# Optimization experiments

Hardware: AMD Instinct MI355X
Metric: run time of the kernel (lower is better)

## Reference

```python
import jax, jax.numpy as jnp
import numpy as np

SEQ, BATCH = 512, 32
VOCAB, HID, FF = 32000, 1024, 4096
HEADS, NX, MAXLEN = 8, 6, 512
EPS = 1e-5


def _full_layer_norm(t):
    # F.layer_norm(t, t.shape): normalize over ALL elements, no affine
    m = jnp.mean(t)
    v = jnp.mean((t - m) ** 2)
    return (t - m) * jax.lax.rsqrt(v + EPS)


def _attention(x, wq, bq, wk, bk, wv, bv, wo, bo):
    # x: [S, B, H]; faithful to the module's quirky reshape:
    # view(B, S//heads, heads, H) splits the SEQUENCE dim across heads,
    # each head keeps the full feature dim H; scores scaled by sqrt(H//heads).
    S, B, H = x.shape
    head_dim = H // HEADS
    q = x @ wq + bq
    k = x @ wk + bk
    v = x @ wv + bv

    def split(t):  # [S,B,H] -> [B, heads, S//heads, H]
        return t.transpose(1, 0, 2).reshape(B, S // HEADS, HEADS, H).transpose(0, 2, 1, 3)

    qh, kh, vh = split(q), split(k), split(v)
    energy = jnp.einsum('bhtf,bhsf->bhts', qh, kh) / np.sqrt(head_dim)
    att = jax.nn.softmax(energy, axis=-1)          # [B, heads, S//h, S//h]
    va = jnp.einsum('bhts,bhsf->bhtf', att, vh)    # [B, heads, S//h, H]
    va = va.transpose(2, 0, 1, 3).reshape(S, B, H)  # back to [S, B, H]
    return va @ wo + bo


def _sub_encoder(x, p, i):
    a = _attention(x, p['wq'][i], p['bq'][i], p['wk'][i], p['bk'][i],
                   p['wv'][i], p['bv'][i], p['wo'][i], p['bo'][i])
    mid = _full_layer_norm(a + x)
    f = jax.nn.relu(mid @ p['w1'][i] + p['b1'][i]) @ p['w2'][i] + p['b2'][i]
    return _full_layer_norm(mid + f)


def setup_inputs() -> dict:
    key = jax.random.key(0)
    ks = jax.random.split(key, 16)
    s = 0.02
    inp = {
        'x': jax.random.randint(ks[0], (SEQ, BATCH), 0, VOCAB),
        'emb': jax.random.normal(ks[1], (VOCAB, HID), jnp.float32) * s,
        'pos_emb': jax.random.normal(ks[2], (MAXLEN, HID), jnp.float32) * s,
        'wq': jax.random.normal(ks[3], (NX, HID, HID), jnp.float32) * s,
        'bq': jnp.zeros((NX, HID), jnp.float32),
        'wk': jax.random.normal(ks[4], (NX, HID, HID), jnp.float32) * s,
        'bk': jnp.zeros((NX, HID), jnp.float32),
        'wv': jax.random.normal(ks[5], (NX, HID, HID), jnp.float32) * s,
        'bv': jnp.zeros((NX, HID), jnp.float32),
        'wo': jax.random.normal(ks[6], (NX, HID, HID), jnp.float32) * s,
        'bo': jnp.zeros((NX, HID), jnp.float32),
        'w1': jax.random.normal(ks[7], (NX, HID, FF), jnp.float32) * s,
        'b1': jnp.zeros((NX, FF), jnp.float32),
        'w2': jax.random.normal(ks[8], (NX, FF, HID), jnp.float32) * s,
        'b2': jnp.zeros((NX, HID), jnp.float32),
    }
    return inp


def reference(x, emb, pos_emb, wq, bq, wk, bk, wv, bv, wo, bo, w1, b1, w2, b2):
    # dropout layers are identity (eval mode); src_mask=None path
    S = x.shape[0]
    p = dict(wq=wq, bq=bq, wk=wk, bk=bk, wv=wv, bv=bv, wo=wo, bo=bo,
             w1=w1, b1=b1, w2=w2, b2=b2)
    h = emb[x] * np.sqrt(HID) + pos_emb[jnp.arange(S)][:, None, :]
    for i in range(NX):
        h = _sub_encoder(h, p, i)
    return h
```

## Files before the change

kernel.cpp:

```cpp
#include <hip/hip_runtime.h>
#include <hip/hip_bf16.h>
#include <stdint.h>

typedef __bf16 bf16_t;
typedef __bf16 bf16x8 __attribute__((ext_vector_type(8)));
typedef __bf16 bf16x4 __attribute__((ext_vector_type(4)));
typedef float  f32x16 __attribute__((ext_vector_type(16)));

#define SEQ   512
#define BATCH 32
#define HID   1024
#define FFD   4096
#define NROW  (SEQ*BATCH)
#define NTOT  ((long)NROW*HID)
#define QKVS  3072

typedef __attribute__((address_space(3))) uint32_t lds_u32;
typedef __attribute__((address_space(1))) const uint32_t glb_u32;

__device__ __forceinline__ void gload_lds16(const void* g, void* l) {
  glb_u32* gp = reinterpret_cast<glb_u32*>(reinterpret_cast<uintptr_t>(g));
  lds_u32* lp = reinterpret_cast<lds_u32*>(reinterpret_cast<uintptr_t>(l));
  __builtin_amdgcn_global_load_lds(gp, lp, 16, 0, 0);
}

__global__ __launch_bounds__(256) void embed_k(const int* __restrict__ x,
    const float* __restrict__ emb, const float* __restrict__ pos,
    bf16_t* __restrict__ hb, float* __restrict__ stId)
{
  if (blockIdx.x == 0 && threadIdx.x == 0) { stId[0] = 0.f; stId[1] = 1.f; }
  const long row = blockIdx.x;
  const int  s   = (int)(row >> 5);
  const long idx = x[row];
  const int  t   = threadIdx.x;
  float4 e  = ((const float4*)(emb + idx*HID))[t];
  float4 pv = ((const float4*)(pos + (long)s*HID))[t];
  bf16x4 ob = {(bf16_t)(e.x*32.f+pv.x), (bf16_t)(e.y*32.f+pv.y),
               (bf16_t)(e.z*32.f+pv.z), (bf16_t)(e.w*32.f+pv.w)};
  *(bf16x4*)(hb + row*HID + (long)t*4) = ob;
}

__device__ __forceinline__ void wcvtNL_body(const float* __restrict__ W,
    bf16_t* __restrict__ wT, int K, int N, int bid)
{
  const int t  = threadIdx.x;
  const int nt = N >> 9;
  const int n  = ((bid % nt) << 9) + t;
  const int k0 = (bid / nt) << 6;
#pragma unroll
  for (int kb = 0; kb < 64; kb += 8) {
    bf16x8 o;
#pragma unroll
    for (int j = 0; j < 8; ++j)
      o[j] = (bf16_t)W[(long)(k0 + kb + j)*N + n];
    *(bf16x8*)&wT[(long)n*K + k0 + kb] = o;
  }
}

__device__ __forceinline__ void csum512_body(const float* __restrict__ W,
    float* __restrict__ out, int K, int N, int bid)
{
  const int n = bid*512 + threadIdx.x;
  float s0 = 0.f, s1 = 0.f, s2 = 0.f, s3 = 0.f;
  for (int k = 0; k < K; k += 4) {
    s0 += W[(long)k*N + n];
    s1 += W[(long)(k+1)*N + n];
    s2 += W[(long)(k+2)*N + n];
    s3 += W[(long)(k+3)*N + n];
  }
  out[n] = (s0 + s1) + (s2 + s3);
}

__global__ __launch_bounds__(512) void prep0(const float* __restrict__ wq,
    const float* __restrict__ wk, const float* __restrict__ wv,
    bf16_t* __restrict__ wT3, float* __restrict__ cs3)
{
  const int b = blockIdx.x;
  if (b < 96) {
    const int sel = b >> 5;
    const float* W = sel == 0 ? wq : sel == 1 ? wk : wv;
    wcvtNL_body(W, wT3 + (size_t)sel*HID*HID, HID, HID, b & 31);
  } else {
    const int col = (b - 96)*512 + threadIdx.x;
    const int sel = col >> 10, n = col & 1023;
    const float* W = sel == 0 ? wq : sel == 1 ? wk : wv;
    float s = 0.f;
    for (int k = 0; k < HID; ++k) s += W[(long)k*HID + n];
    cs3[col] = s;
  }
}

template<int MODE, int PREP>
__global__ __launch_bounds__(512, 4)
void gemmW(const bf16_t* __restrict__ A, const bf16_t* __restrict__ Bt,
           const float* __restrict__ ba, const float* __restrict__ bb,
           const float* __restrict__ bc, const float* __restrict__ cs,
           const float* __restrict__ stats, const bf16_t* __restrict__ res,
           bf16_t* __restrict__ outB, float* __restrict__ part,
           int M, int N, int K, int P,
           const float* __restrict__ pw0, bf16_t* __restrict__ pd0,
           const float* __restrict__ pw1, const float* __restrict__ pw2,
           const float* __restrict__ pw3, bf16_t* __restrict__ pd1,
           float* __restrict__ pf0)
{
  __shared__ bf16_t As[128][64];
  __shared__ bf16_t Bs[256][64];
  __shared__ float  rs[512], rq[512];
  const int tid = threadIdx.x;

  if (PREP > 0 && (int)blockIdx.x < P) {
    const int b = blockIdx.x;
    if (PREP == 1) {
      if (b < 32) wcvtNL_body(pw0, pd0, 1024, 1024, b);
      else        csum512_body(pw1, pf0, 1024, 4096, b - 32);
    } else if (PREP == 2) {
      wcvtNL_body(pw0, pd0, 1024, 4096, b);
    } else if (PREP == 3) {
      if (b < 128)      wcvtNL_body(pw0, pd0, 4096, 1024, b);
      else if (b < 160) wcvtNL_body(pw1, pd1, 1024, 1024, b-128);
      else if (b < 192) wcvtNL_body(pw2, pd1 + (size_t)HID*HID, 1024, 1024, b-160);
      else if (b < 224) wcvtNL_body(pw3, pd1 + (size_t)2*HID*HID, 1024, 1024, b-192);
      else {
        const int col = (b - 224)*512 + tid;
        const int sel = col >> 10, n = col & 1023;
        const float* W = sel == 0 ? pw1 : sel == 1 ? pw2 : pw3;
        float s = 0.f;
        for (int k = 0; k < HID; ++k) s += W[(long)k*HID + n];
        pf0[col] = s;
      }
    }
    return;
  }
  const int gbid = blockIdx.x - P;

  const int w = tid >> 6, l = tid & 63;
  const int wm = w >> 2, wn = w & 3;
  const int lr = l & 31, hi = l >> 5;

  const int nbn = N >> 8;
  const int nwg = gridDim.x - P;
  const int q8 = nwg >> 3, r8 = nwg & 7;
  const int xcd = gbid & 7, bidx = gbid >> 3;
  const int wg = (xcd < r8 ? xcd*(q8+1) : r8*(q8+1) + (xcd-r8)*q8) + bidx;
  const long bm = wg / nbn, bn = wg % nbn;
  const long rA0 = bm << 7, rB0 = bn << 8;

  const int srow   = tid >> 3;
  const int schunk = (((tid & 7) ^ ((tid >> 3) & 7)) << 3);
  const int ldsw   = (tid >> 6) << 10;

  f32x16 a00 = {0}, a01 = {0}, a10 = {0}, a11 = {0};

#define STG_TILE(kt) do { \
    const long kb_ = (long)(kt)*64 + schunk; \
    gload_lds16(A  + (rA0 + srow)*(long)K + kb_,        (char*)As + ldsw); \
    gload_lds16(A  + (rA0 + 64 + srow)*(long)K + kb_,   (char*)As + 8192 + ldsw); \
    gload_lds16(Bt + (rB0 + srow)*(long)K + kb_,        (char*)Bs + ldsw); \
    gload_lds16(Bt + (rB0 + 64 + srow)*(long)K + kb_,   (char*)Bs + 8192 + ldsw); \
    gload_lds16(Bt + (rB0 + 128 + srow)*(long)K + kb_,  (char*)Bs + 16384 + ldsw); \
    gload_lds16(Bt + (rB0 + 192 + srow)*(long)K + kb_,  (char*)Bs + 24576 + ldsw); \
  } while (0)
#define FRA(mt, kk) (*(const bf16x8*)((const char*)As + (wm*64 + (mt)*32 + lr)*128 + \
                      ((((kk)*2 + hi) ^ (l & 7)) << 4)))
#define FRB(nt, kk) (*(const bf16x8*)((const char*)Bs + (wn*64 + (nt)*32 + lr)*128 + \
                      ((((kk)*2 + hi) ^ (l & 7)) << 4)))

  const int nk = K >> 6;
  for (int t = 0; t < nk; ++t) {
    __syncthreads();
    STG_TILE(t);
    __syncthreads();
#pragma unroll
    for (int kk = 0; kk < 4; ++kk) {
      bf16x8 fa0 = FRA(0, kk), fa1 = FRA(1, kk);
      bf16x8 fb0 = FRB(0, kk), fb1 = FRB(1, kk);
      a00 = __builtin_amdgcn_mfma_f32_32x32x16_bf16(fa0, fb0, a00, 0, 0, 0);
      a01 = __builtin_amdgcn_mfma_f32_32x32x16_bf16(fa0, fb1, a01, 0, 0, 0);
      a10 = __builtin_amdgcn_mfma_f32_32x32x16_bf16(fa1, fb0, a10, 0, 0, 0);
      a11 = __builtin_amdgcn_mfma_f32_32x32x16_bf16(fa1, fb1, a11, 0, 0, 0);
    }
  }
#undef STG_TILE
#undef FRA
#undef FRB

  const float mS = stats[0], rS = stats[1];
  const bool q3 = (N == 3072);
  float ls = 0.f, lsq = 0.f;
  const long rowT = rA0 + wm*64 + 4*hi;
  const long colT = rB0 + wn*64 + lr;
#pragma unroll
  for (int nt = 0; nt < 2; ++nt) {
    const long col = colT + nt*32;
    float bv;
    if (MODE == 3 && q3)
      bv = col < 1024 ? ba[col] : col < 2048 ? bb[col - 1024] : bc[col - 2048];
    else
      bv = ba[col];
    float beta = 0.f;
    if (MODE == 3 || MODE == 4) beta = bv - mS*rS*cs[col];
#pragma unroll
    for (int mt = 0; mt < 2; ++mt) {
      const f32x16 acc = mt == 0 ? (nt == 0 ? a00 : a01) : (nt == 0 ? a10 : a11);
#pragma unroll
      for (int r = 0; r < 16; ++r) {
        const long row = rowT + mt*32 + (r & 3) + 8*(r >> 2);
        const long off = row*(long)N + col;
        float v;
        if (MODE == 3)      v = fmaf(acc[r], rS, beta);
        else if (MODE == 4) v = fmaxf(fmaf(acc[r], rS, beta), 0.f);
        else {
          v = acc[r] + bv + ((float)res[off] - mS)*rS;
          ls += v; lsq += v*v;
        }
        outB[off] = (bf16_t)v;
      }
    }
  }
  if (MODE == 5) {
    rs[tid] = ls; rq[tid] = lsq;
    __syncthreads();
    for (int o = 256; o > 0; o >>= 1) {
      if (tid < o) { rs[tid] += rs[tid+o]; rq[tid] += rq[tid+o]; }
      __syncthreads();
    }
    if (tid == 0) { part[2*gbid] = rs[0]; part[2*gbid + 1] = rq[0]; }
  }
}

__global__ __launch_bounds__(256) void attn_k(
    const bf16_t* __restrict__ qkv, bf16_t* __restrict__ ob)
{
  __shared__ __align__(16) char smem[64*128*2*2 + 64*64*4 + 64*4];
  bf16_t* Qc = (bf16_t*)smem;
  bf16_t* Kc = (bf16_t*)(smem + 16384);
  bf16_t* Vc = (bf16_t*)smem;
  float*  E    = (float*)(smem + 32768);
  float*  Rinv = (float*)(smem + 49152);

  const int tid  = threadIdx.x;
  const int head = blockIdx.x & 7, b = blockIdx.x >> 3;
  const long rbase = (long)head*32 + b;

  const int ti = tid >> 2, g = tid & 3;
  const int lr  = tid >> 2;
  const int lp0 = (tid & 3) * 4;

  float eacc[16];
#pragma unroll
  for (int j = 0; j < 16; ++j) eacc[j] = 0.f;

  for (int kc = 0; kc < HID; kc += 128) {
    __syncthreads();
    const bf16_t* qrow = qkv + (lr*256 + rbase)*QKVS + kc;
    const bf16_t* krow = qkv + (lr*256 + rbase)*QKVS + 1024 + kc;
#pragma unroll
    for (int i = 0; i < 4; ++i) {
      const int p = lp0 + i;
      const int src = (p ^ (lr & 7)) * 8;
      *(uint4*)&Qc[lr*128 + p*8] = *(const uint4*)&qrow[src];
      *(uint4*)&Kc[lr*128 + p*8] = *(const uint4*)&krow[src];
    }
    __syncthreads();
    for (int e8 = 0; e8 < 16; ++e8) {
      const int qp = e8 ^ (ti & 7);
      bf16x8 qv = *(bf16x8*)&Qc[ti*128 + qp*8];
      float qf[8];
#pragma unroll
      for (int u = 0; u < 8; ++u) qf[u] = (float)qv[u];
#pragma unroll
      for (int j = 0; j < 16; ++j) {
        const int s  = j*4 + g;
        const int kp = e8 ^ (s & 7);
        bf16x8 kv = *(bf16x8*)&Kc[s*128 + kp*8];
        float a = eacc[j];
#pragma unroll
        for (int u = 0; u < 8; ++u) a += qf[u] * (float)kv[u];
        eacc[j] = a;
      }
    }
  }
  const float scale = 0.0883883476483184f;
  float mx = -1e30f;
#pragma unroll
  for (int j = 0; j < 16; ++j) { eacc[j] *= scale; mx = fmaxf(mx, eacc[j]); }
  mx = fmaxf(mx, __shfl_xor(mx, 1));
  mx = fmaxf(mx, __shfl_xor(mx, 2));
  float sum = 0.f;
#pragma unroll
  for (int j = 0; j < 16; ++j) {
    const float pj = __expf(eacc[j] - mx);
    E[(j*4 + g)*64 + ti] = pj;
    sum += pj;
  }
  sum += __shfl_xor(sum, 1);
  sum += __shfl_xor(sum, 2);
  if (g == 0) Rinv[ti] = 1.f / sum;
  __syncthreads();

  const int lane = tid & 63, wq_ = tid >> 6;
  const float rv = Rinv[lane];
  const long orow = (long)lane*256 + b*8 + head;
  for (int fc = 0; fc < HID; fc += 128) {
    __syncthreads();
    const bf16_t* vrow = qkv + (lr*256 + rbase)*QKVS + 2048 + fc;
#pragma unroll
    for (int i = 0; i < 4; ++i) {
      const int p = lp0 + i;
      *(uint4*)&Vc[lr*128 + p*8] = *(const uint4*)&vrow[p*8];
    }
    __syncthreads();
    float vacc[32];
#pragma unroll
    for (int u = 0; u < 32; ++u) vacc[u] = 0.f;
    for (int s = 0; s < 64; ++s) {
      const float pp = E[s*64 + lane];
#pragma unroll
      for (int u = 0; u < 4; ++u) {
        bf16x8 vv = *(bf16x8*)&Vc[s*128 + wq_*32 + u*8];
#pragma unroll
        for (int t8 = 0; t8 < 8; ++t8) vacc[u*8 + t8] += pp * (float)vv[t8];
      }
    }
#pragma unroll
    for (int u = 0; u < 4; ++u) {
      bf16x8 ov;
#pragma unroll
      for (int t8 = 0; t8 < 8; ++t8) ov[t8] = (bf16_t)(vacc[u*8 + t8] * rv);
      *(bf16x8*)&ob[orow*HID + fc + wq_*32 + u*8] = ov;
    }
  }
}

__global__ __launch_bounds__(256) void reduce2(const float* __restrict__ part,
                                               float* __restrict__ stats, int np)
{
  __shared__ double sh[256], sh2[256];
  const int tid = threadIdx.x;
  double s = 0.0, s2 = 0.0;
  for (int i = tid; i < np; i += 256) { s += part[2*i]; s2 += part[2*i + 1]; }
  sh[tid] = s; sh2[tid] = s2; __syncthreads();
  for (int o = 128; o > 0; o >>= 1) {
    if (tid < o) { sh[tid] += sh[tid+o]; sh2[tid] += sh2[tid+o]; }
    __syncthreads();
  }
  if (tid == 0) {
    const double n = (double)NTOT;
    const double mean = sh[0] / n;
    const double var  = sh2[0] / n - mean*mean;
    stats[0] = (float)mean;
    stats[1] = (float)(1.0 / sqrt(var + 1e-5));
  }
}

__global__ __launch_bounds__(256) void final_norm(const bf16_t* __restrict__ t,
    const float* __restrict__ stats, float* __restrict__ out)
{
  const float m = stats[0], r = stats[1];
  const long n8 = NTOT / 8;
  for (long i = (long)blockIdx.x*blockDim.x + threadIdx.x; i < n8;
       i += (long)gridDim.x*blockDim.x) {
    bf16x8 v = ((const bf16x8*)t)[i];
    float4 o0 = {((float)v[0]-m)*r, ((float)v[1]-m)*r, ((float)v[2]-m)*r, ((float)v[3]-m)*r};
    float4 o1 = {((float)v[4]-m)*r, ((float)v[5]-m)*r, ((float)v[6]-m)*r, ((float)v[7]-m)*r};
    ((float4*)out)[2*i]   = o0;
    ((float4*)out)[2*i+1] = o1;
  }
}

extern "C" void kernel_launch(void* const* d_in, const int* in_sizes, int n_in,
                              void* d_out, int out_size, void* d_ws, size_t ws_size,
                              hipStream_t stream)
{
  const int*   x    = (const int*)  d_in[0];
  const float* emb  = (const float*)d_in[1];
  const float* pos  = (const float*)d_in[2];
  const float* wq_a = (const float*)d_in[3];
  const float* bq_a = (const float*)d_in[4];
  const float* wk_a = (const float*)d_in[5];
  const float* bk_a = (const float*)d_in[6];
  const float* wv_a = (const float*)d_in[7];
  const float* bv_a = (const float*)d_in[8];
  const float* wo_a = (const float*)d_in[9];
  const float* bo_a = (const float*)d_in[10];
  const float* w1_a = (const float*)d_in[11];
  const float* b1_a = (const float*)d_in[12];
  const float* w2_a = (const float*)d_in[13];
  const float* b2_a = (const float*)d_in[14];

  char* p = (char*)d_ws;
  auto take = [&](size_t n) { char* r = p; p += (n + 255) & ~(size_t)255; return r; };
  bf16_t* hb   = (bf16_t*)take(NTOT*2);
  bf16_t* U    = (bf16_t*)take((size_t)NROW*FFD*2);
  bf16_t* qkv  = U;
  bf16_t* attb = U + 3*NTOT;
  bf16_t* ffb  = U;
  bf16_t* wTo  = (bf16_t*)take((size_t)HID*HID*2);
  bf16_t* wT1  = (bf16_t*)take((size_t)HID*FFD*2);
  bf16_t* wT2  = (bf16_t*)take((size_t)HID*FFD*2);
  bf16_t* wT3  = (bf16_t*)take((size_t)3*HID*HID*2);
  float*  cs1  = (float*) take(FFD*4);
  float*  cs3  = (float*) take(QKVS*4);
  float*  part = (float*) take(4096*4);
  float*  stId = (float*) take(256);
  float*  st1  = (float*) take(256);
  float*  st2  = (float*) take(256);

  const int gQKV = (NROW/128)*(QKVS/256);
  const int gH   = (NROW/128)*(HID/256);
  const int gF   = (NROW/128)*(FFD/256);

  embed_k<<<NROW, 256, 0, stream>>>(x, emb, pos, hb, stId);
  prep0<<<102, 512, 0, stream>>>(wq_a, wk_a, wv_a, wT3, cs3);

  for (int i = 0; i < 6; ++i) {
    const float* Bq = bq_a + (size_t)i*HID;
    const float* Bk = bk_a + (size_t)i*HID;
    const float* Bv = bv_a + (size_t)i*HID;
    const float* Wo = wo_a + (size_t)i*HID*HID;  const float* Bo = bo_a + (size_t)i*HID;
    const float* W1 = w1_a + (size_t)i*HID*FFD;  const float* B1 = b1_a + (size_t)i*FFD;
    const float* W2 = w2_a + (size_t)i*FFD*HID;  const float* B2 = b2_a + (size_t)i*HID;
    const float* stIn = (i == 0) ? stId : st2;
    const int haveNext = (i < 5);
    const float* Wqn = wq_a + (size_t)(i+1)*HID*HID;
    const float* Wkn = wk_a + (size_t)(i+1)*HID*HID;
    const float* Wvn = wv_a + (size_t)(i+1)*HID*HID;

    gemmW<3,1><<<40 + gQKV, 512, 0, stream>>>(
        hb, wT3, Bq, Bk, Bv, cs3, stIn, nullptr, qkv, nullptr,
        NROW, QKVS, HID, 40, Wo, wTo, W1, nullptr, nullptr, nullptr, cs1);

    attn_k<<<256, 256, 0, stream>>>(qkv, attb);

    gemmW<5,2><<<128 + gH, 512, 0, stream>>>(
        attb, wTo, Bo, Bo, Bo, nullptr, stIn, hb, hb, part,
        NROW, HID, HID, 128, W1, wT1, nullptr, nullptr, nullptr, nullptr, nullptr);
    reduce2<<<1, 256, 0, stream>>>(part, st1, gH);

    const int P3 = haveNext ? 230 : 128;
    gemmW<4,3><<<P3 + gF, 512, 0, stream>>>(
        hb, wT1, B1, B1, B1, cs1, st1, nullptr, ffb, nullptr,
        NROW, FFD, HID, P3, W2, wT2, Wqn, Wkn, Wvn, wT3, cs3);

    gemmW<5,0><<<gH, 512, 0, stream>>>(
        ffb, wT2, B2, B2, B2, nullptr, st1, hb, hb, part,
        NROW, HID, FFD, 0, nullptr, nullptr, nullptr, nullptr, nullptr, nullptr, nullptr);
    reduce2<<<1, 256, 0, stream>>>(part, st2, gH);
  }

  final_norm<<<2048, 256, 0, stream>>>(hb, st2, (float*)d_out);
}
```

Before: 4.198 ms.

## Move weight prep into a standalone kernel and widen attention to 512 threads

Weight conversion and transposition, plus column sums, were previously spread as extra prep blocks across the GEMM launches. They now run in a single prep kernel launched after attention. This removes the prep branch and blockIdx offset from the GEMM kernel, and the prep work no longer competes with or imbalances the GEMM tiles. The attention kernel now uses 512 threads, each handling half as many score columns and output features, with an XOR swizzle on the probability buffer in shared memory to avoid bank conflicts. The cost is one extra kernel launch and less register work per thread.

```diff
diff --git a/kernel.cpp b/kernel.cpp
--- a/kernel.cpp
+++ b/kernel.cpp
@@ -90,57 +90,54 @@
   }
 }
 
-template<int MODE, int PREP>
+__global__ __launch_bounds__(512) void prep_k(
+    const float* __restrict__ Wo, bf16_t* __restrict__ wTo,
+    const float* __restrict__ W1, bf16_t* __restrict__ wT1, float* __restrict__ cs1,
+    const float* __restrict__ W2, bf16_t* __restrict__ wT2,
+    const float* __restrict__ Wq, const float* __restrict__ Wk,
+    const float* __restrict__ Wv, bf16_t* __restrict__ wT3,
+    float* __restrict__ cs3)
+{
+  const int b = blockIdx.x;
+  if (b < 32)        wcvtNL_body(Wo, wTo, HID, HID, b);
+  else if (b < 160)  wcvtNL_body(W1, wT1, HID, FFD, b - 32);
+  else if (b < 288)  wcvtNL_body(W2, wT2, FFD, HID, b - 160);
+  else if (b < 296)  csum512_body(W1, cs1, HID, FFD, b - 288);
+  else if (b < 392) {
+    const int i = b - 296, sel = i >> 5;
+    const float* W = sel == 0 ? Wq : sel == 1 ? Wk : Wv;
+    wcvtNL_body(W, wT3 + (size_t)sel*HID*HID, HID, HID, i & 31);
+  } else {
+    const int col = (b - 392)*512 + threadIdx.x;
+    const int sel = col >> 10, n = col & 1023;
+    const float* W = sel == 0 ? Wq : sel == 1 ? Wk : Wv;
+    float s = 0.f;
+    for (int k = 0; k < HID; ++k) s += W[(long)k*HID + n];
+    cs3[col] = s;
+  }
+}
+
+template<int MODE>
 __global__ __launch_bounds__(512, 4)
 void gemmW(const bf16_t* __restrict__ A, const bf16_t* __restrict__ Bt,
            const float* __restrict__ ba, const float* __restrict__ bb,
            const float* __restrict__ bc, const float* __restrict__ cs,
            const float* __restrict__ stats, const bf16_t* __restrict__ res,
            bf16_t* __restrict__ outB, float* __restrict__ part,
-           int M, int N, int K, int P,
-           const float* __restrict__ pw0, bf16_t* __restrict__ pd0,
-           const float* __restrict__ pw1, const float* __restrict__ pw2,
-           const float* __restrict__ pw3, bf16_t* __restrict__ pd1,
-           float* __restrict__ pf0)
+           int M, int N, int K)
 {
   __shared__ bf16_t As[128][64];
   __shared__ bf16_t Bs[256][64];
   __shared__ float  rs[512], rq[512];
   const int tid = threadIdx.x;
-
-  if (PREP > 0 && (int)blockIdx.x < P) {
-    const int b = blockIdx.x;
-    if (PREP == 1) {
-      if (b < 32) wcvtNL_body(pw0, pd0, 1024, 1024, b);
-      else        csum512_body(pw1, pf0, 1024, 4096, b - 32);
-    } else if (PREP == 2) {
-      wcvtNL_body(pw0, pd0, 1024, 4096, b);
-    } else if (PREP == 3) {
-      if (b < 128)      wcvtNL_body(pw0, pd0, 4096, 1024, b);
-      else if (b < 160) wcvtNL_body(pw1, pd1, 1024, 1024, b-128);
-      else if (b < 192) wcvtNL_body(pw2, pd1 + (size_t)HID*HID, 1024, 1024, b-160);
-      else if (b < 224) wcvtNL_body(pw3, pd1 + (size_t)2*HID*HID, 1024, 1024, b-192);
-      else {
-        const int col = (b - 224)*512 + tid;
-        const int sel = col >> 10, n = col & 1023;
-        const float* W = sel == 0 ? pw1 : sel == 1 ? pw2 : pw3;
-        float s = 0.f;
-        for (int k = 0; k < HID; ++k) s += W[(long)k*HID + n];
-        pf0[col] = s;
-      }
-    }
-    return;
-  }
-  const int gbid = blockIdx.x - P;
-
   const int w = tid >> 6, l = tid & 63;
   const int wm = w >> 2, wn = w & 3;
   const int lr = l & 31, hi = l >> 5;
 
   const int nbn = N >> 8;
-  const int nwg = gridDim.x - P;
+  const int nwg = gridDim.x;
   const int q8 = nwg >> 3, r8 = nwg & 7;
-  const int xcd = gbid & 7, bidx = gbid >> 3;
+  const int xcd = blockIdx.x & 7, bidx = blockIdx.x >> 3;
   const int wg = (xcd < r8 ? xcd*(q8+1) : r8*(q8+1) + (xcd-r8)*q8) + bidx;
   const long bm = wg / nbn, bn = wg % nbn;
   const long rA0 = bm << 7, rB0 = bn << 8;
@@ -224,11 +221,11 @@
       if (tid < o) { rs[tid] += rs[tid+o]; rq[tid] += rq[tid+o]; }
       __syncthreads();
     }
-    if (tid == 0) { part[2*gbid] = rs[0]; part[2*gbid + 1] = rq[0]; }
-  }
-}
-
-__global__ __launch_bounds__(256) void attn_k(
+    if (tid == 0) { part[2*blockIdx.x] = rs[0]; part[2*blockIdx.x + 1] = rq[0]; }
+  }
+}
+
+__global__ __launch_bounds__(512) void attn_k(
     const bf16_t* __restrict__ qkv, bf16_t* __restrict__ ob)
 {
   __shared__ __align__(16) char smem[64*128*2*2 + 64*64*4 + 64*4];
@@ -242,21 +239,20 @@
   const int head = blockIdx.x & 7, b = blockIdx.x >> 3;
   const long rbase = (long)head*32 + b;
 
-  const int ti = tid >> 2, g = tid & 3;
-  const int lr  = tid >> 2;
-  const int lp0 = (tid & 3) * 4;
-
-  float eacc[16];
-#pragma unroll
-  for (int j = 0; j < 16; ++j) eacc[j] = 0.f;
+  const int ti = tid >> 3, g = tid & 7;
+  const int lr = tid >> 3;
+
+  float eacc[8];
+#pragma unroll
+  for (int j = 0; j < 8; ++j) eacc[j] = 0.f;
 
   for (int kc = 0; kc < HID; kc += 128) {
     __syncthreads();
     const bf16_t* qrow = qkv + (lr*256 + rbase)*QKVS + kc;
     const bf16_t* krow = qkv + (lr*256 + rbase)*QKVS + 1024 + kc;
 #pragma unroll
-    for (int i = 0; i < 4; ++i) {
-      const int p = lp0 + i;
+    for (int i = 0; i < 2; ++i) {
+      const int p = i*8 + g;
       const int src = (p ^ (lr & 7)) * 8;
       *(uint4*)&Qc[lr*128 + p*8] = *(const uint4*)&qrow[src];
       *(uint4*)&Kc[lr*128 + p*8] = *(const uint4*)&krow[src];
@@ -269,8 +265,8 @@
 #pragma unroll
       for (int u = 0; u < 8; ++u) qf[u] = (float)qv[u];
 #pragma unroll
-      for (int j = 0; j < 16; ++j) {
-        const int s  = j*4 + g;
+      for (int j = 0; j < 8; ++j) {
+        const int s  = j*8 + g;
         const int kp = e8 ^ (s & 7);
         bf16x8 kv = *(bf16x8*)&Kc[s*128 + kp*8];
         float a = eacc[j];
@@ -283,51 +279,54 @@
   const float scale = 0.0883883476483184f;
   float mx = -1e30f;
 #pragma unroll
-  for (int j = 0; j < 16; ++j) { eacc[j] *= scale; mx = fmaxf(mx, eacc[j]); }
+  for (int j = 0; j < 8; ++j) { eacc[j] *= scale; mx = fmaxf(mx, eacc[j]); }
   mx = fmaxf(mx, __shfl_xor(mx, 1));
   mx = fmaxf(mx, __shfl_xor(mx, 2));
+  mx = fmaxf(mx, __shfl_xor(mx, 4));
   float sum = 0.f;
 #pragma unroll
-  for (int j = 0; j < 16; ++j) {
+  for (int j = 0; j < 8; ++j) {
     const float pj = __expf(eacc[j] - mx);
-    E[(j*4 + g)*64 + ti] = pj;
+    const int s = j*8 + g;
+    E[s*64 + (ti ^ (s & 7))] = pj;
     sum += pj;
   }
   sum += __shfl_xor(sum, 1);
   sum += __shfl_xor(sum, 2);
+  sum += __shfl_xor(sum, 4);
   if (g == 0) Rinv[ti] = 1.f / sum;
   __syncthreads();
 
-  const int lane = tid & 63, wq_ = tid >> 6;
+  const int lane = tid & 63, w8 = tid >> 6;
   const float rv = Rinv[lane];
   const long orow = (long)lane*256 + b*8 + head;
   for (int fc = 0; fc < HID; fc += 128) {
     __syncthreads();
     const bf16_t* vrow = qkv + (lr*256 + rbase)*QKVS + 2048 + fc;
 #pragma unroll
-    for (int i = 0; i < 4; ++i) {
-      const int p = lp0 + i;
+    for (int i = 0; i < 2; ++i) {
+      const int p = i*8 + g;
       *(uint4*)&Vc[lr*128 + p*8] = *(const uint4*)&vrow[p*8];
     }
     __syncthreads();
-    float vacc[32];
-#pragma unroll
-    for (int u = 0; u < 32; ++u) vacc[u] = 0.f;
+    float vacc[16];
+#pragma unroll
+    for (int u = 0; u < 16; ++u) vacc[u] = 0.f;
     for (int s = 0; s < 64; ++s) {
-      const float pp = E[s*64 + lane];
-#pragma unroll
-      for (int u = 0; u < 4; ++u) {
-        bf16x8 vv = *(bf16x8*)&Vc[s*128 + wq_*32 + u*8];
+      const float pp = E[s*64 + (lane ^ (s & 7))];
+#pragma unroll
+      for (int u = 0; u < 2; ++u) {
+        bf16x8 vv = *(bf16x8*)&Vc[s*128 + w8*16 + u*8];
 #pragma unroll
         for (int t8 = 0; t8 < 8; ++t8) vacc[u*8 + t8] += pp * (float)vv[t8];
       }
     }
 #pragma unroll
-    for (int u = 0; u < 4; ++u) {
+    for (int u = 0; u < 2; ++u) {
       bf16x8 ov;
 #pragma unroll
       for (int t8 = 0; t8 < 8; ++t8) ov[t8] = (bf16_t)(vacc[u*8 + t8] * rv);
-      *(bf16x8*)&ob[orow*HID + fc + wq_*32 + u*8] = ov;
+      *(bf16x8*)&ob[orow*HID + fc + w8*16 + u*8] = ov;
     }
   }
 }
@@ -426,25 +425,23 @@
     const float* Wkn = wk_a + (size_t)(i+1)*HID*HID;
     const float* Wvn = wv_a + (size_t)(i+1)*HID*HID;
 
-    gemmW<3,1><<<40 + gQKV, 512, 0, stream>>>(
-        hb, wT3, Bq, Bk, Bv, cs3, stIn, nullptr, qkv, nullptr,
-        NROW, QKVS, HID, 40, Wo, wTo, W1, nullptr, nullptr, nullptr, cs1);
-
-    attn_k<<<256, 256, 0, stream>>>(qkv, attb);
-
-    gemmW<5,2><<<128 + gH, 512, 0, stream>>>(
-        attb, wTo, Bo, Bo, Bo, nullptr, stIn, hb, hb, part,
-        NROW, HID, HID, 128, W1, wT1, nullptr, nullptr, nullptr, nullptr, nullptr);
+    gemmW<3><<<gQKV, 512, 0, stream>>>(hb, wT3, Bq, Bk, Bv, cs3, stIn,
+                                       nullptr, qkv, nullptr, NROW, QKVS, HID);
+
+    attn_k<<<256, 512, 0, stream>>>(qkv, attb);
+
+    prep_k<<<haveNext ? 398 : 296, 512, 0, stream>>>(
+        Wo, wTo, W1, wT1, cs1, W2, wT2, Wqn, Wkn, Wvn, wT3, cs3);
+
+    gemmW<5><<<gH, 512, 0, stream>>>(attb, wTo, Bo, Bo, Bo, nullptr, stIn,
+                                     hb, hb, part, NROW, HID, HID);
     reduce2<<<1, 256, 0, stream>>>(part, st1, gH);
 
-    const int P3 = haveNext ? 230 : 128;
-    gemmW<4,3><<<P3 + gF, 512, 0, stream>>>(
-        hb, wT1, B1, B1, B1, cs1, st1, nullptr, ffb, nullptr,
-        NROW, FFD, HID, P3, W2, wT2, Wqn, Wkn, Wvn, wT3, cs3);
-
-    gemmW<5,0><<<gH, 512, 0, stream>>>(
-        ffb, wT2, B2, B2, B2, nullptr, st1, hb, hb, part,
-        NROW, HID, FFD, 0, nullptr, nullptr, nullptr, nullptr, nullptr, nullptr, nullptr);
+    gemmW<4><<<gF, 512, 0, stream>>>(hb, wT1, B1, B1, B1, cs1, st1,
+                                     nullptr, ffb, nullptr, NROW, FFD, HID);
+
+    gemmW<5><<<gH, 512, 0, stream>>>(ffb, wT2, B2, B2, B2, nullptr, st1,
+                                     hb, hb, part, NROW, HID, FFD);
     reduce2<<<1, 256, 0, stream>>>(part, st2, gH);
   }
 
```

Result: faster. 4.054 ms (-3.4%).
